# Optimization experiments

Measured on AMD Instinct MI355X. Metric: run time of the kernel, lower is better.

## Reference

```python
import jax, jax.numpy as jnp
import numpy as np

B, S, E, H, FFN, NQ = 4, 2048, 1024, 16, 4096, 8
DK = E // H
EPS = 1e-5


def setup_inputs() -> dict:
    key = jax.random.key(0)
    ks = jax.random.split(key, 8)
    x = jax.random.normal(ks[0], (B, S, E), dtype=jnp.float32)
    theta = jax.random.normal(ks[1], (NQ,), dtype=jnp.float32)  # RY angles
    w1 = jax.random.normal(ks[2], (FFN, NQ), dtype=jnp.float32) / np.sqrt(NQ)
    b1 = jnp.zeros((FFN,), dtype=jnp.float32)
    w2 = jax.random.normal(ks[3], (E, FFN), dtype=jnp.float32) / np.sqrt(FFN)
    b2 = jnp.zeros((E,), dtype=jnp.float32)
    gamma1 = jnp.ones((E,), dtype=jnp.float32)
    beta1 = jnp.zeros((E,), dtype=jnp.float32)
    gamma2 = jnp.ones((E,), dtype=jnp.float32)
    beta2 = jnp.zeros((E,), dtype=jnp.float32)
    return {"x": x, "theta": theta, "w1": w1, "b1": b1, "w2": w2, "b2": b2,
            "gamma1": gamma1, "beta1": beta1, "gamma2": gamma2, "beta2": beta2}


def _layernorm(h, g, b):
    mu = jnp.mean(h, axis=-1, keepdims=True)
    var = jnp.mean(jnp.square(h - mu), axis=-1, keepdims=True)
    return (h - mu) * jax.lax.rsqrt(var + EPS) * g + b


def _attention(x):
    # q = k = v = separate_heads(x); no projection weights in the original.
    q = x.reshape(B, S, H, DK).transpose(0, 2, 1, 3)  # [B,H,S,DK]
    scores = jnp.einsum("bhqd,bhkd->bhqk", q, q) / np.sqrt(DK)
    probs = jax.nn.softmax(scores, axis=-1)
    out = jnp.einsum("bhqk,bhkd->bhqd", probs, q)
    return out.transpose(0, 2, 1, 3).reshape(B, S, E)


def _ffn_quantum(h, theta, w1, b1, w2, b2):
    # Per-token circuit: RX(x_i) then RY(theta_i) on independent qubits,
    # measure PauliZ -> <Z_i> = cos(x_i) * cos(theta_i). Batched over all tokens.
    qout = jnp.cos(h[..., :NQ]) * jnp.cos(theta)  # [B,S,NQ]
    hid = jax.nn.relu(jnp.einsum("bsq,fq->bsf", qout, w1) + b1)
    return jnp.einsum("bsf,ef->bse", hid, w2) + b2


def reference(x, theta, w1, b1, w2, b2, gamma1, beta1, gamma2, beta2):
    attn_out = _attention(x)
    h = _layernorm(x + attn_out, gamma1, beta1)
    ffn_out = _ffn_quantum(h, theta, w1, b1, w2, b2)
    return _layernorm(h + ffn_out, gamma2, beta2)
```

## Files before the change

kernel.cpp:

```cpp
#include <hip/hip_runtime.h>


#define Bq 4
#define Sq 2048
#define Eq 1024
#define Hq 16
#define DKq 64
#define FFNq 4096
#define NQq 8
#define LOG2E 1.44269504f

typedef unsigned int u32;
typedef unsigned short u16;
typedef _Float16 f16;
typedef f16 f16x8 __attribute__((ext_vector_type(8)));
typedef __fp16 fp16x2 __attribute__((ext_vector_type(2)));
typedef float f32x4 __attribute__((ext_vector_type(4)));

#if __has_builtin(__builtin_amdgcn_exp2f)
#define EXP2F __builtin_amdgcn_exp2f
#else
#define EXP2F exp2f
#endif

#define MFMA(a, b, c) __builtin_amdgcn_mfma_f32_16x16x32_f16((a), (b), (c), 0, 0, 0)

#define GLL(g, l)                                                          \
  __builtin_amdgcn_global_load_lds(                                        \
      (const __attribute__((address_space(1))) u32*)(g),                   \
      (__attribute__((address_space(3))) u32*)(l), 16, 0, 0)

__device__ __forceinline__ u16 f2h(float x) {
  f16 t = (f16)x;
  return __builtin_bit_cast(u16, t);
}
__device__ __forceinline__ float h2f(u16 w) {
  return (float)__builtin_bit_cast(f16, w);
}
#if __has_builtin(__builtin_amdgcn_cvt_pkrtz)
__device__ __forceinline__ u32 pkrtz(float a, float b) {
  fp16x2 r = __builtin_amdgcn_cvt_pkrtz(a, b);
  return __builtin_bit_cast(u32, r);
}
#else
__device__ __forceinline__ u32 pkrtz(float a, float b) {
  return (u32)f2h(a) | ((u32)f2h(b) << 16);
}
#endif

union F8 { f16x8 v; u32 w[4]; u16 h[8]; f16 e[8]; };

__global__ void k_cvt(const float* __restrict__ src, uint4* __restrict__ dst, int n8) {
  int i = blockIdx.x * 256 + threadIdx.x;
  if (i >= n8) return;
  const float4* s = (const float4*)src + 2 * (long)i;
  float4 a = s[0], b = s[1];
  uint4 r;
  r.x = pkrtz(a.x, a.y);
  r.y = pkrtz(a.z, a.w);
  r.z = pkrtz(b.x, b.y);
  r.w = pkrtz(b.z, b.w);
  dst[i] = r;
}

__global__ void k_prep(const float* __restrict__ x, u16* __restrict__ xh,
                       u16* __restrict__ xt) {
  __shared__ u16 tile[64 * 72];
  const int tid = threadIdx.x;
  const int bx = blockIdx.x;
  const int sb = bx & 31, bh = bx >> 5;
  const int b = bh >> 4, h = bh & 15;
  const int s0 = sb * 64;
  const int r = tid >> 2, cq = tid & 3;
  const float* xp = x + ((long)(b * Sq + s0 + r)) * Eq + h * 64 + cq * 16;
  float4 f0 = ((const float4*)xp)[0], f1 = ((const float4*)xp)[1];
  float4 f2 = ((const float4*)xp)[2], f3 = ((const float4*)xp)[3];
  u32 w[8];
  w[0] = pkrtz(f0.x, f0.y); w[1] = pkrtz(f0.z, f0.w);
  w[2] = pkrtz(f1.x, f1.y); w[3] = pkrtz(f1.z, f1.w);
  w[4] = pkrtz(f2.x, f2.y); w[5] = pkrtz(f2.z, f2.w);
  w[6] = pkrtz(f3.x, f3.y); w[7] = pkrtz(f3.z, f3.w);
  uint4* xo = (uint4*)(xh + ((long)(b * Sq + s0 + r)) * Eq + h * 64 + cq * 16);
  xo[0] = make_uint4(w[0], w[1], w[2], w[3]);
  xo[1] = make_uint4(w[4], w[5], w[6], w[7]);
  uint4* tp = (uint4*)(tile + r * 72 + cq * 16);
  tp[0] = make_uint4(w[0], w[1], w[2], w[3]);
  tp[1] = make_uint4(w[4], w[5], w[6], w[7]);
  __syncthreads();
  const int d = tid >> 2, rq = tid & 3;
  u32 o[8];
#pragma unroll
  for (int i = 0; i < 8; ++i) {
    u32 lo = tile[(rq * 16 + 2 * i) * 72 + d];
    u32 hi = tile[(rq * 16 + 2 * i + 1) * 72 + d];
    o[i] = lo | (hi << 16);
  }
  uint4* to = (uint4*)(xt + ((long)(bh * 64 + d)) * Sq + s0 + rq * 16);
  to[0] = make_uint4(o[0], o[1], o[2], o[3]);
  to[1] = make_uint4(o[4], o[5], o[6], o[7]);
}

__global__ __launch_bounds__(256, 2) void k_attn(const u16* __restrict__ xh,
                                                 const u16* __restrict__ xt,
                                                 u16* __restrict__ attn) {
  __shared__ __align__(16) u16 lds[32768];
  u16* Pl = lds + 16384;

  const int tid = threadIdx.x;
  const int wave = tid >> 6, lane = tid & 63;
  const int n = lane & 15, quad = lane >> 4;

  const int bx = blockIdx.x;
  const int qb = bx >> 6, bh = bx & 63;
  const int b = bh >> 4, h = bh & 15;

  const u16* xh_bh = xh + (long)b * Sq * Eq + h * 64;
  const u16* xt_bh = xt + (long)bh * 64 * Sq;

  const float SC = 0.125f * LOG2E;
  F8 qf[4][2];
  float shift[4], lrow[4] = {0.f, 0.f, 0.f, 0.f};
#pragma unroll
  for (int nt = 0; nt < 4; ++nt) {
    const int q = qb * 256 + wave * 64 + nt * 16 + n;
    const u16* qp = xh_bh + (long)q * Eq + quad * 8;
    F8 a, c;
    a.v = *(const f16x8*)qp;
    c.v = *(const f16x8*)(qp + 32);
    float s2 = 0.f;
#pragma unroll
    for (int i = 0; i < 8; ++i) {
      float va = (float)a.e[i], vc = (float)c.e[i];
      s2 += va * va + vc * vc;
      qf[nt][0].e[i] = a.e[i] * (f16)SC;
      qf[nt][1].e[i] = c.e[i] * (f16)SC;
    }
    s2 += __shfl_xor(s2, 16);
    s2 += __shfl_xor(s2, 32);
    shift[nt] = SC * s2;
  }

  const int r8 = lane >> 3;
  const int cl = (lane & 7) ^ r8;
  const u16* gK0 = xh_bh + (long)(wave * 16 + r8) * Eq + cl * 8;
  const u16* gK1 = gK0 + 8 * Eq;
  const u16* gV0 = xt_bh + (long)(wave * 16 + r8) * Sq + cl * 8;
  const u16* gV1 = gV0 + 8 * Sq;
  const int lK0 = wave * 1024, lK1 = lK0 + 512;
  const int lV0 = 4096 + wave * 1024, lV1 = lV0 + 512;

  u16* cur = lds;
  u16* nxt = lds + 8192;

  GLL(gK0, cur + lK0); GLL(gK1, cur + lK1);
  GLL(gV0, cur + lV0); GLL(gV1, cur + lV1);
  gK0 += 64 * Eq; gK1 += 64 * Eq; gV0 += 64; gV1 += 64;

  f32x4 O[4][4] = {};
  u16* Pw = Pl + wave * 4096;

  for (int kb = 0; kb < Sq / 64; ++kb) {
    __syncthreads();
    if (kb < Sq / 64 - 1) {
      GLL(gK0, nxt + lK0); GLL(gK1, nxt + lK1);
      GLL(gV0, nxt + lV0); GLL(gV1, nxt + lV1);
      gK0 += 64 * Eq; gK1 += 64 * Eq; gV0 += 64; gV1 += 64;
    }
    u16* Kl = cur;
    u16* Vt = cur + 4096;

    f32x4 ST[4][4];
#pragma unroll
    for (int nt = 0; nt < 4; ++nt) {
      const float ms = -shift[nt];
#pragma unroll
      for (int mt = 0; mt < 4; ++mt) {
        ST[nt][mt][0] = ms; ST[nt][mt][1] = ms;
        ST[nt][mt][2] = ms; ST[nt][mt][3] = ms;
      }
    }
#pragma unroll
    for (int mt = 0; mt < 4; ++mt) {
#pragma unroll
      for (int c = 0; c < 2; ++c) {
        f16x8 af = *(const f16x8*)(Kl + (mt * 16 + n) * 64 +
                                   (((c * 4 + quad) ^ (n & 7)) * 8));
#pragma unroll
        for (int nt = 0; nt < 4; ++nt)
          ST[nt][mt] = MFMA(af, qf[nt][c].v, ST[nt][mt]);
      }
    }

#pragma unroll
    for (int nt = 0; nt < 4; ++nt) {
      float ls = 0.f;
#pragma unroll
      for (int mt = 0; mt < 4; ++mt) {
        float p0 = EXP2F(ST[nt][mt][0]);
        float p1 = EXP2F(ST[nt][mt][1]);
        float p2 = EXP2F(ST[nt][mt][2]);
        float p3 = EXP2F(ST[nt][mt][3]);
        ls += (p0 + p1) + (p2 + p3);
        const int ch = 2 * mt + (quad >> 1);
        *(uint2*)(Pw + nt * 1024 + n * 64 + ((ch ^ (n & 7)) * 8) + (quad & 1) * 4) =
            make_uint2(pkrtz(p0, p1), pkrtz(p2, p3));
      }
      lrow[nt] += ls;
    }

#pragma unroll
    for (int c = 0; c < 2; ++c) {
      const int pc = ((c * 4 + quad) ^ (n & 7)) * 8;
      f16x8 pf[4];
#pragma unroll
      for (int nt = 0; nt < 4; ++nt)
        pf[nt] = *(const f16x8*)(Pw + nt * 1024 + n * 64 + pc);
#pragma unroll
      for (int dt = 0; dt < 4; ++dt) {
        f16x8 vf = *(const f16x8*)(Vt + (dt * 16 + n) * 64 + pc);
#pragma unroll
        for (int nt = 0; nt < 4; ++nt) O[nt][dt] = MFMA(vf, pf[nt], O[nt][dt]);
      }
    }
    u16* t = cur; cur = nxt; nxt = t;
  }

#pragma unroll
  for (int nt = 0; nt < 4; ++nt) {
    float l = lrow[nt];
    l += __shfl_xor(l, 16);
    l += __shfl_xor(l, 32);
    const float inv = 1.0f / l;
    const int q = qb * 256 + wave * 64 + nt * 16 + n;
    u16* op = attn + (long)b * Sq * Eq + (long)q * Eq + h * 64;
#pragma unroll
    for (int dt = 0; dt < 4; ++dt) {
      u32 w0 = pkrtz(O[nt][dt][0] * inv, O[nt][dt][1] * inv);
      u32 w1 = pkrtz(O[nt][dt][2] * inv, O[nt][dt][3] * inv);
      *(uint2*)(op + dt * 16 + quad * 4) = make_uint2(w0, w1);
    }
  }
}

__global__ void k_ln1(const u16* __restrict__ xh, const u16* __restrict__ attn,
                      const float* __restrict__ g, const float* __restrict__ be,
                      const float* __restrict__ theta, u16* __restrict__ hout,
                      u16* __restrict__ qout) {
  const long t = blockIdx.x;
  const int tid = threadIdx.x;
  uint2 xw = ((const uint2*)(xh + t * Eq))[tid];
  uint2 aw = ((const uint2*)(attn + t * Eq))[tid];
  float v0 = h2f(xw.x & 0xffff) + h2f(aw.x & 0xffff);
  float v1 = h2f(xw.x >> 16) + h2f(aw.x >> 16);
  float v2 = h2f(xw.y & 0xffff) + h2f(aw.y & 0xffff);
  float v3 = h2f(xw.y >> 16) + h2f(aw.y >> 16);
  float s = (v0 + v1) + (v2 + v3);
  float s2 = v0 * v0 + v1 * v1 + v2 * v2 + v3 * v3;
#pragma unroll
  for (int o = 1; o < 64; o <<= 1) {
    s += __shfl_xor(s, o);
    s2 += __shfl_xor(s2, o);
  }
  __shared__ float red[8];
  const int wv = tid >> 6, ln = tid & 63;
  if (ln == 0) { red[wv] = s; red[4 + wv] = s2; }
  __syncthreads();
  s = red[0] + red[1] + red[2] + red[3];
  s2 = red[4] + red[5] + red[6] + red[7];
  const float mu = s * (1.f / Eq);
  const float var = s2 * (1.f / Eq) - mu * mu;
  const float rstd = rsqrtf(var + 1e-5f);
  float4 gv = ((const float4*)g)[tid];
  float4 bv = ((const float4*)be)[tid];
  float o0 = (v0 - mu) * rstd * gv.x + bv.x;
  float o1 = (v1 - mu) * rstd * gv.y + bv.y;
  float o2 = (v2 - mu) * rstd * gv.z + bv.z;
  float o3 = (v3 - mu) * rstd * gv.w + bv.w;
  ((uint2*)(hout + t * Eq))[tid] = make_uint2(pkrtz(o0, o1), pkrtz(o2, o3));
  if (tid < 2) {
    float hv[4] = {o0, o1, o2, o3};
    float q[4];
#pragma unroll
    for (int i = 0; i < 4; ++i) q[i] = cosf(hv[i]) * cosf(theta[tid * 4 + i]);
    *(uint2*)(qout + t * NQq + tid * 4) = make_uint2(pkrtz(q[0], q[1]), pkrtz(q[2], q[3]));
  }
}

__global__ void k_hid(const u16* __restrict__ qout, const float* __restrict__ w1,
                      const float* __restrict__ b1, u16* __restrict__ hid) {
  __shared__ float qs[256][8];
  const int tid = threadIdx.x;
  const int fb = blockIdx.x & 63, tb = blockIdx.x >> 6;
  const int f0 = fb * 64, t0 = tb * 256;
  {
    uint4 qw = *(const uint4*)(qout + (long)(t0 + tid) * NQq);
    qs[tid][0] = h2f(qw.x & 0xffff); qs[tid][1] = h2f(qw.x >> 16);
    qs[tid][2] = h2f(qw.y & 0xffff); qs[tid][3] = h2f(qw.y >> 16);
    qs[tid][4] = h2f(qw.z & 0xffff); qs[tid][5] = h2f(qw.z >> 16);
    qs[tid][6] = h2f(qw.w & 0xffff); qs[tid][7] = h2f(qw.w >> 16);
  }
  __syncthreads();
  const int wave = tid >> 6, lane = tid & 63;
  const int f = f0 + lane;
  const float4* wp = (const float4*)(w1 + (long)f * NQq);
  float4 wa = wp[0], wb = wp[1];
  const float bb = b1[f];
  const int trow = wave * 64;
  u16* op = hid + (long)(t0 + trow) * FFNq + f;
#pragma unroll 4
  for (int i = 0; i < 64; ++i) {
    const float* q = qs[trow + i];
    float acc = bb + q[0] * wa.x + q[1] * wa.y + q[2] * wa.z + q[3] * wa.w +
                q[4] * wb.x + q[5] * wb.y + q[6] * wb.z + q[7] * wb.w;
    acc = fmaxf(acc, 0.f);
    op[(long)i * FFNq] = f2h(acc);
  }
}

__global__ __launch_bounds__(256, 2) void k_gemm(const u16* __restrict__ Ah,
                                                 const u16* __restrict__ Bh,
                                                 u16* __restrict__ C) {
  __shared__ __align__(16) u16 lds[32768];
  const int tid = threadIdx.x;
  const int wave = tid >> 6, lane = tid & 63;
  const int n = lane & 15, quad = lane >> 4;
  const int wm = wave >> 1, wn = wave & 1;
  const int m0 = (blockIdx.x >> 3) * 128;
  const int n0 = (blockIdx.x & 7) * 128;
  const int r8 = lane >> 3;
  const int cl = (lane & 7) ^ r8;

  const u16* gA[4];
  const u16* gB[4];
  int lA[4], lB[4];
#pragma unroll
  for (int j = 0; j < 4; ++j) {
    const int row = wave * 32 + j * 8;
    gA[j] = Ah + (long)(m0 + row + r8) * FFNq + cl * 8;
    gB[j] = Bh + (long)(n0 + row + r8) * FFNq + cl * 8;
    lA[j] = row * 64;
    lB[j] = 8192 + row * 64;
  }

  u16* cur = lds;
  u16* nxt = lds + 16384;

#pragma unroll
  for (int j = 0; j < 4; ++j) {
    GLL(gA[j], cur + lA[j]);
    GLL(gB[j], cur + lB[j]);
    gA[j] += 64;
    gB[j] += 64;
  }

  f32x4 acc[4][4] = {};
  for (int it = 0; it < FFNq / 64; ++it) {
    __syncthreads();
    if (it < FFNq / 64 - 1) {
#pragma unroll
      for (int j = 0; j < 4; ++j) {
        GLL(gA[j], nxt + lA[j]);
        GLL(gB[j], nxt + lB[j]);
        gA[j] += 64;
        gB[j] += 64;
      }
    }
    u16* La = cur;
    u16* Lb = cur + 8192;
#pragma unroll
    for (int c = 0; c < 2; ++c) {
      f16x8 af[4], bf[4];
#pragma unroll
      for (int i = 0; i < 4; ++i) {
        const int ra = wm * 64 + i * 16 + n;
        const int rb = wn * 64 + i * 16 + n;
        af[i] = *(const f16x8*)(La + ra * 64 + (((c * 4 + quad) ^ (n & 7)) * 8));
        bf[i] = *(const f16x8*)(Lb + rb * 64 + (((c * 4 + quad) ^ (n & 7)) * 8));
      }
#pragma unroll
      for (int i = 0; i < 4; ++i)
#pragma unroll
        for (int j = 0; j < 4; ++j) acc[i][j] = MFMA(af[i], bf[j], acc[i][j]);
    }
    u16* t = cur; cur = nxt; nxt = t;
  }
#pragma unroll
  for (int i = 0; i < 4; ++i) {
    const int row = m0 + wm * 64 + i * 16 + quad * 4;
#pragma unroll
    for (int j = 0; j < 4; ++j) {
      u16* cp = C + (long)row * Eq + n0 + wn * 64 + j * 16 + n;
      cp[0] = f2h(acc[i][j][0]);
      cp[Eq] = f2h(acc[i][j][1]);
      cp[2 * Eq] = f2h(acc[i][j][2]);
      cp[3 * Eq] = f2h(acc[i][j][3]);
    }
  }
}

__global__ void k_ln2(const u16* __restrict__ hin, const u16* __restrict__ ffn,
                      const float* __restrict__ b2, const float* __restrict__ g,
                      const float* __restrict__ be, float* __restrict__ out) {
  const long t = blockIdx.x;
  const int tid = threadIdx.x;
  uint2 hw = ((const uint2*)(hin + t * Eq))[tid];
  uint2 fw = ((const uint2*)(ffn + t * Eq))[tid];
  float4 b2v = ((const float4*)b2)[tid];
  float v0 = h2f(hw.x & 0xffff) + h2f(fw.x & 0xffff) + b2v.x;
  float v1 = h2f(hw.x >> 16) + h2f(fw.x >> 16) + b2v.y;
  float v2 = h2f(hw.y & 0xffff) + h2f(fw.y & 0xffff) + b2v.z;
  float v3 = h2f(hw.y >> 16) + h2f(fw.y >> 16) + b2v.w;
  float s = (v0 + v1) + (v2 + v3);
  float s2 = v0 * v0 + v1 * v1 + v2 * v2 + v3 * v3;
#pragma unroll
  for (int o = 1; o < 64; o <<= 1) {
    s += __shfl_xor(s, o);
    s2 += __shfl_xor(s2, o);
  }
  __shared__ float red[8];
  const int wv = tid >> 6, ln = tid & 63;
  if (ln == 0) { red[wv] = s; red[4 + wv] = s2; }
  __syncthreads();
  s = red[0] + red[1] + red[2] + red[3];
  s2 = red[4] + red[5] + red[6] + red[7];
  const float mu = s * (1.f / Eq);
  const float var = s2 * (1.f / Eq) - mu * mu;
  const float rstd = rsqrtf(var + 1e-5f);
  float4 gv = ((const float4*)g)[tid];
  float4 bv = ((const float4*)be)[tid];
  float4 o;
  o.x = (v0 - mu) * rstd * gv.x + bv.x;
  o.y = (v1 - mu) * rstd * gv.y + bv.y;
  o.z = (v2 - mu) * rstd * gv.z + bv.z;
  o.w = (v3 - mu) * rstd * gv.w + bv.w;
  ((float4*)(out + t * Eq))[tid] = o;
}

extern "C" void kernel_launch(void* const* d_in, const int* in_sizes, int n_in,
                              void* d_out, int out_size, void* d_ws, size_t ws_size,
                              hipStream_t stream) {
  const float* x = (const float*)d_in[0];
  const float* theta = (const float*)d_in[1];
  const float* w1 = (const float*)d_in[2];
  const float* b1 = (const float*)d_in[3];
  const float* w2 = (const float*)d_in[4];
  const float* b2 = (const float*)d_in[5];
  const float* g1 = (const float*)d_in[6];
  const float* be1 = (const float*)d_in[7];
  const float* g2 = (const float*)d_in[8];
  const float* be2 = (const float*)d_in[9];
  float* out = (float*)d_out;

  char* ws = (char*)d_ws;
  u16* attn = (u16*)(ws);
  u16* h = (u16*)(ws + 16777216);
  u16* xh = (u16*)(ws + 33554432);
  u16* xt = (u16*)(ws + 50331648);
  u16* ffn = (u16*)(ws + 67108864);
  u16* hid = (u16*)(ws + 83886080);
  u16* w2h = (u16*)(ws + 150994944);
  u16* qout = (u16*)(ws + 159383552);

  k_prep<<<Bq * Hq * (Sq / 64), 256, 0, stream>>>(x, xh, xt);
  k_cvt<<<2048, 256, 0, stream>>>(w2, (uint4*)w2h, (Eq * FFNq) / 8);
  k_attn<<<Bq * Hq * (Sq / 256), 256, 0, stream>>>(xh, xt, attn);
  k_ln1<<<Bq * Sq, 256, 0, stream>>>(xh, attn, g1, be1, theta, h, qout);
  k_hid<<<(Bq * Sq / 256) * (FFNq / 64), 256, 0, stream>>>(qout, w1, b1, hid);
  k_gemm<<<(Bq * Sq / 128) * (Eq / 128), 256, 0, stream>>>(hid, w2h, ffn);
  k_ln2<<<Bq * Sq, 256, 0, stream>>>(h, ffn, b2, g2, be2, out);
}
```

Measured before the change: 316.9 us.

## Replace global_load_lds with register-staged prefetch and compute row sums via MFMA

Both the attention and FFN GEMM kernels stop using direct global-to-LDS loads. They now load the next tile into registers before the compute phase and write it to LDS after the compute, a classic register-staged double buffer. The attention kernel also drops the per-thread exp sum and the shuffle reductions, computing softmax row sums with an extra MFMA against a ones vector. This trades more registers, which may cut occupancy, and extra VALU/LDS store instructions for different load/compute overlap.

```diff
diff --git a/kernel.cpp b/kernel.cpp
--- a/kernel.cpp
+++ b/kernel.cpp
@@ -24,11 +24,6 @@
 #endif
 
 #define MFMA(a, b, c) __builtin_amdgcn_mfma_f32_16x16x32_f16((a), (b), (c), 0, 0, 0)
-
-#define GLL(g, l)                                                          \
-  __builtin_amdgcn_global_load_lds(                                        \
-      (const __attribute__((address_space(1))) u32*)(g),                   \
-      (__attribute__((address_space(3))) u32*)(l), 16, 0, 0)
 
 __device__ __forceinline__ u16 f2h(float x) {
   f16 t = (f16)x;
@@ -119,7 +114,7 @@
 
   const float SC = 0.125f * LOG2E;
   F8 qf[4][2];
-  float shift[4], lrow[4] = {0.f, 0.f, 0.f, 0.f};
+  float shift[4];
 #pragma unroll
   for (int nt = 0; nt < 4; ++nt) {
     const int q = qb * 256 + wave * 64 + nt * 16 + n;
@@ -146,24 +141,35 @@
   const u16* gK1 = gK0 + 8 * Eq;
   const u16* gV0 = xt_bh + (long)(wave * 16 + r8) * Sq + cl * 8;
   const u16* gV1 = gV0 + 8 * Sq;
-  const int lK0 = wave * 1024, lK1 = lK0 + 512;
-  const int lV0 = 4096 + wave * 1024, lV1 = lV0 + 512;
+  const int lK0 = wave * 1024 + lane * 8;
+  const int lK1 = lK0 + 512;
+  const int lV0 = 4096 + wave * 1024 + lane * 8;
+  const int lV1 = lV0 + 512;
 
   u16* cur = lds;
   u16* nxt = lds + 8192;
 
-  GLL(gK0, cur + lK0); GLL(gK1, cur + lK1);
-  GLL(gV0, cur + lV0); GLL(gV1, cur + lV1);
-  gK0 += 64 * Eq; gK1 += 64 * Eq; gV0 += 64; gV1 += 64;
+  {
+    uint4 sK0 = *(const uint4*)gK0, sK1 = *(const uint4*)gK1;
+    uint4 sV0 = *(const uint4*)gV0, sV1 = *(const uint4*)gV1;
+    gK0 += 64 * Eq; gK1 += 64 * Eq; gV0 += 64; gV1 += 64;
+    *(uint4*)(cur + lK0) = sK0; *(uint4*)(cur + lK1) = sK1;
+    *(uint4*)(cur + lV0) = sV0; *(uint4*)(cur + lV1) = sV1;
+  }
 
   f32x4 O[4][4] = {};
+  f32x4 lC[4] = {};
+  const f16x8 vones = {(f16)1, (f16)1, (f16)1, (f16)1,
+                       (f16)1, (f16)1, (f16)1, (f16)1};
   u16* Pw = Pl + wave * 4096;
 
   for (int kb = 0; kb < Sq / 64; ++kb) {
     __syncthreads();
-    if (kb < Sq / 64 - 1) {
-      GLL(gK0, nxt + lK0); GLL(gK1, nxt + lK1);
-      GLL(gV0, nxt + lV0); GLL(gV1, nxt + lV1);
+    const bool pre = kb < Sq / 64 - 1;
+    uint4 sK0, sK1, sV0, sV1;
+    if (pre) {
+      sK0 = *(const uint4*)gK0; sK1 = *(const uint4*)gK1;
+      sV0 = *(const uint4*)gV0; sV1 = *(const uint4*)gV1;
       gK0 += 64 * Eq; gK1 += 64 * Eq; gV0 += 64; gV1 += 64;
     }
     u16* Kl = cur;
@@ -193,19 +199,16 @@
 
 #pragma unroll
     for (int nt = 0; nt < 4; ++nt) {
-      float ls = 0.f;
 #pragma unroll
       for (int mt = 0; mt < 4; ++mt) {
         float p0 = EXP2F(ST[nt][mt][0]);
         float p1 = EXP2F(ST[nt][mt][1]);
         float p2 = EXP2F(ST[nt][mt][2]);
         float p3 = EXP2F(ST[nt][mt][3]);
-        ls += (p0 + p1) + (p2 + p3);
         const int ch = 2 * mt + (quad >> 1);
         *(uint2*)(Pw + nt * 1024 + n * 64 + ((ch ^ (n & 7)) * 8) + (quad & 1) * 4) =
             make_uint2(pkrtz(p0, p1), pkrtz(p2, p3));
       }
-      lrow[nt] += ls;
     }
 
 #pragma unroll
@@ -213,8 +216,10 @@
       const int pc = ((c * 4 + quad) ^ (n & 7)) * 8;
       f16x8 pf[4];
 #pragma unroll
-      for (int nt = 0; nt < 4; ++nt)
+      for (int nt = 0; nt < 4; ++nt) {
         pf[nt] = *(const f16x8*)(Pw + nt * 1024 + n * 64 + pc);
+        lC[nt] = MFMA(vones, pf[nt], lC[nt]);
+      }
 #pragma unroll
       for (int dt = 0; dt < 4; ++dt) {
         f16x8 vf = *(const f16x8*)(Vt + (dt * 16 + n) * 64 + pc);
@@ -222,15 +227,17 @@
         for (int nt = 0; nt < 4; ++nt) O[nt][dt] = MFMA(vf, pf[nt], O[nt][dt]);
       }
     }
+
+    if (pre) {
+      *(uint4*)(nxt + lK0) = sK0; *(uint4*)(nxt + lK1) = sK1;
+      *(uint4*)(nxt + lV0) = sV0; *(uint4*)(nxt + lV1) = sV1;
+    }
     u16* t = cur; cur = nxt; nxt = t;
   }
 
 #pragma unroll
   for (int nt = 0; nt < 4; ++nt) {
-    float l = lrow[nt];
-    l += __shfl_xor(l, 16);
-    l += __shfl_xor(l, 32);
-    const float inv = 1.0f / l;
+    const float inv = 1.0f / lC[nt][0];
     const int q = qb * 256 + wave * 64 + nt * 16 + n;
     u16* op = attn + (long)b * Sq * Eq + (long)q * Eq + h * 64;
 #pragma unroll
@@ -338,29 +345,39 @@
     const int row = wave * 32 + j * 8;
     gA[j] = Ah + (long)(m0 + row + r8) * FFNq + cl * 8;
     gB[j] = Bh + (long)(n0 + row + r8) * FFNq + cl * 8;
-    lA[j] = row * 64;
-    lB[j] = 8192 + row * 64;
+    lA[j] = row * 64 + lane * 8;
+    lB[j] = 8192 + row * 64 + lane * 8;
   }
 
   u16* cur = lds;
   u16* nxt = lds + 16384;
 
-#pragma unroll
-  for (int j = 0; j < 4; ++j) {
-    GLL(gA[j], cur + lA[j]);
-    GLL(gB[j], cur + lB[j]);
-    gA[j] += 64;
-    gB[j] += 64;
+  {
+    uint4 sA[4], sB[4];
+#pragma unroll
+    for (int j = 0; j < 4; ++j) {
+      sA[j] = *(const uint4*)gA[j];
+      sB[j] = *(const uint4*)gB[j];
+      gA[j] += 64;
+      gB[j] += 64;
+    }
+#pragma unroll
+    for (int j = 0; j < 4; ++j) {
+      *(uint4*)(cur + lA[j]) = sA[j];
+      *(uint4*)(cur + lB[j]) = sB[j];
+    }
   }
 
   f32x4 acc[4][4] = {};
   for (int it = 0; it < FFNq / 64; ++it) {
     __syncthreads();
-    if (it < FFNq / 64 - 1) {
+    const bool pre = it < FFNq / 64 - 1;
+    uint4 sA[4], sB[4];
+    if (pre) {
 #pragma unroll
       for (int j = 0; j < 4; ++j) {
-        GLL(gA[j], nxt + lA[j]);
-        GLL(gB[j], nxt + lB[j]);
+        sA[j] = *(const uint4*)gA[j];
+        sB[j] = *(const uint4*)gB[j];
         gA[j] += 64;
         gB[j] += 64;
       }
@@ -381,6 +398,13 @@
       for (int i = 0; i < 4; ++i)
 #pragma unroll
         for (int j = 0; j < 4; ++j) acc[i][j] = MFMA(af[i], bf[j], acc[i][j]);
+    }
+    if (pre) {
+#pragma unroll
+      for (int j = 0; j < 4; ++j) {
+        *(uint4*)(nxt + lA[j]) = sA[j];
+        *(uint4*)(nxt + lB[j]) = sB[j];
+      }
     }
     u16* t = cur; cur = nxt; nxt = t;
   }
```

New measurement: 425.6 us. 34.3% more time.

## Shrink attention query tile, split-K the FFN GEMM, single-buffer LDS

Applied to the files above, without the earlier changes.

The attention kernel now gives each block 128 queries instead of 256 and each wave 2 query tiles instead of 4. It drops the double-buffered K/V LDS staging in favor of a single buffer with two barriers per iteration, and computes softmax row sums with an extra MFMA against a vector of ones instead of scalar adds and shuffles. The FFN output GEMM is split along K into two halves that write separate partial buffers, and the second LayerNorm adds the two partials. The goal is to double the number of blocks and cut LDS and register use per block, raising occupancy and filling the CUs better. The cost is that global loads no longer overlap compute within a block, each iteration adds a barrier, and the GEMM writes and reads an extra fp16 partial buffer.

```diff
diff --git a/kernel.cpp b/kernel.cpp
--- a/kernel.cpp
+++ b/kernel.cpp
@@ -100,11 +100,13 @@
   to[1] = make_uint4(o[4], o[5], o[6], o[7]);
 }
 
-__global__ __launch_bounds__(256, 2) void k_attn(const u16* __restrict__ xh,
-                                                 const u16* __restrict__ xt,
-                                                 u16* __restrict__ attn) {
-  __shared__ __align__(16) u16 lds[32768];
-  u16* Pl = lds + 16384;
+__global__ __launch_bounds__(256) void k_attn(const u16* __restrict__ xh,
+                                              const u16* __restrict__ xt,
+                                              u16* __restrict__ attn) {
+  __shared__ __align__(16) u16 lds[16384];
+  u16* Kl = lds;
+  u16* Vt = lds + 4096;
+  u16* Pl = lds + 8192;
 
   const int tid = threadIdx.x;
   const int wave = tid >> 6, lane = tid & 63;
@@ -118,11 +120,11 @@
   const u16* xt_bh = xt + (long)bh * 64 * Sq;
 
   const float SC = 0.125f * LOG2E;
-  F8 qf[4][2];
-  float shift[4], lrow[4] = {0.f, 0.f, 0.f, 0.f};
-#pragma unroll
-  for (int nt = 0; nt < 4; ++nt) {
-    const int q = qb * 256 + wave * 64 + nt * 16 + n;
+  F8 qf[2][2];
+  float shift[2];
+#pragma unroll
+  for (int nt = 0; nt < 2; ++nt) {
+    const int q = qb * 128 + wave * 32 + nt * 16 + n;
     const u16* qp = xh_bh + (long)q * Eq + quad * 8;
     F8 a, c;
     a.v = *(const f16x8*)qp;
@@ -146,32 +148,28 @@
   const u16* gK1 = gK0 + 8 * Eq;
   const u16* gV0 = xt_bh + (long)(wave * 16 + r8) * Sq + cl * 8;
   const u16* gV1 = gV0 + 8 * Sq;
-  const int lK0 = wave * 1024, lK1 = lK0 + 512;
-  const int lV0 = 4096 + wave * 1024, lV1 = lV0 + 512;
-
-  u16* cur = lds;
-  u16* nxt = lds + 8192;
-
-  GLL(gK0, cur + lK0); GLL(gK1, cur + lK1);
-  GLL(gV0, cur + lV0); GLL(gV1, cur + lV1);
-  gK0 += 64 * Eq; gK1 += 64 * Eq; gV0 += 64; gV1 += 64;
-
-  f32x4 O[4][4] = {};
-  u16* Pw = Pl + wave * 4096;
+  u16* lK0 = Kl + wave * 1024;
+  u16* lK1 = lK0 + 512;
+  u16* lV0 = Vt + wave * 1024;
+  u16* lV1 = lV0 + 512;
+
+  f32x4 O[2][4] = {};
+  f32x4 lC[2] = {};
+  const f16x8 vones = {(f16)1, (f16)1, (f16)1, (f16)1,
+                       (f16)1, (f16)1, (f16)1, (f16)1};
+  u16* Pw0 = Pl + (wave * 2 + 0) * 1024;
+  u16* Pw1 = Pl + (wave * 2 + 1) * 1024;
 
   for (int kb = 0; kb < Sq / 64; ++kb) {
     __syncthreads();
-    if (kb < Sq / 64 - 1) {
-      GLL(gK0, nxt + lK0); GLL(gK1, nxt + lK1);
-      GLL(gV0, nxt + lV0); GLL(gV1, nxt + lV1);
-      gK0 += 64 * Eq; gK1 += 64 * Eq; gV0 += 64; gV1 += 64;
-    }
-    u16* Kl = cur;
-    u16* Vt = cur + 4096;
-
-    f32x4 ST[4][4];
-#pragma unroll
-    for (int nt = 0; nt < 4; ++nt) {
+    GLL(gK0, lK0); GLL(gK1, lK1);
+    GLL(gV0, lV0); GLL(gV1, lV1);
+    gK0 += 64 * Eq; gK1 += 64 * Eq; gV0 += 64; gV1 += 64;
+    __syncthreads();
+
+    f32x4 ST[2][4];
+#pragma unroll
+    for (int nt = 0; nt < 2; ++nt) {
       const float ms = -shift[nt];
 #pragma unroll
       for (int mt = 0; mt < 4; ++mt) {
@@ -185,53 +183,46 @@
       for (int c = 0; c < 2; ++c) {
         f16x8 af = *(const f16x8*)(Kl + (mt * 16 + n) * 64 +
                                    (((c * 4 + quad) ^ (n & 7)) * 8));
-#pragma unroll
-        for (int nt = 0; nt < 4; ++nt)
-          ST[nt][mt] = MFMA(af, qf[nt][c].v, ST[nt][mt]);
+        ST[0][mt] = MFMA(af, qf[0][c].v, ST[0][mt]);
+        ST[1][mt] = MFMA(af, qf[1][c].v, ST[1][mt]);
       }
     }
 
 #pragma unroll
-    for (int nt = 0; nt < 4; ++nt) {
-      float ls = 0.f;
+    for (int nt = 0; nt < 2; ++nt) {
+      u16* Pw = nt ? Pw1 : Pw0;
 #pragma unroll
       for (int mt = 0; mt < 4; ++mt) {
         float p0 = EXP2F(ST[nt][mt][0]);
         float p1 = EXP2F(ST[nt][mt][1]);
         float p2 = EXP2F(ST[nt][mt][2]);
         float p3 = EXP2F(ST[nt][mt][3]);
-        ls += (p0 + p1) + (p2 + p3);
         const int ch = 2 * mt + (quad >> 1);
-        *(uint2*)(Pw + nt * 1024 + n * 64 + ((ch ^ (n & 7)) * 8) + (quad & 1) * 4) =
+        *(uint2*)(Pw + n * 64 + ((ch ^ (n & 7)) * 8) + (quad & 1) * 4) =
             make_uint2(pkrtz(p0, p1), pkrtz(p2, p3));
       }
-      lrow[nt] += ls;
     }
 
 #pragma unroll
     for (int c = 0; c < 2; ++c) {
       const int pc = ((c * 4 + quad) ^ (n & 7)) * 8;
-      f16x8 pf[4];
-#pragma unroll
-      for (int nt = 0; nt < 4; ++nt)
-        pf[nt] = *(const f16x8*)(Pw + nt * 1024 + n * 64 + pc);
+      f16x8 pf0 = *(const f16x8*)(Pw0 + n * 64 + pc);
+      f16x8 pf1 = *(const f16x8*)(Pw1 + n * 64 + pc);
+      lC[0] = MFMA(vones, pf0, lC[0]);
+      lC[1] = MFMA(vones, pf1, lC[1]);
 #pragma unroll
       for (int dt = 0; dt < 4; ++dt) {
         f16x8 vf = *(const f16x8*)(Vt + (dt * 16 + n) * 64 + pc);
-#pragma unroll
-        for (int nt = 0; nt < 4; ++nt) O[nt][dt] = MFMA(vf, pf[nt], O[nt][dt]);
+        O[0][dt] = MFMA(vf, pf0, O[0][dt]);
+        O[1][dt] = MFMA(vf, pf1, O[1][dt]);
       }
     }
-    u16* t = cur; cur = nxt; nxt = t;
-  }
-
-#pragma unroll
-  for (int nt = 0; nt < 4; ++nt) {
-    float l = lrow[nt];
-    l += __shfl_xor(l, 16);
-    l += __shfl_xor(l, 32);
-    const float inv = 1.0f / l;
-    const int q = qb * 256 + wave * 64 + nt * 16 + n;
+  }
+
+#pragma unroll
+  for (int nt = 0; nt < 2; ++nt) {
+    const float inv = 1.0f / lC[nt][0];
+    const int q = qb * 128 + wave * 32 + nt * 16 + n;
     u16* op = attn + (long)b * Sq * Eq + (long)q * Eq + h * 64;
 #pragma unroll
     for (int dt = 0; dt < 4; ++dt) {
@@ -317,56 +308,50 @@
   }
 }
 
-__global__ __launch_bounds__(256, 2) void k_gemm(const u16* __restrict__ Ah,
-                                                 const u16* __restrict__ Bh,
-                                                 u16* __restrict__ C) {
-  __shared__ __align__(16) u16 lds[32768];
+__global__ __launch_bounds__(256) void k_gemm(const u16* __restrict__ Ah,
+                                              const u16* __restrict__ Bh,
+                                              u16* __restrict__ C0,
+                                              u16* __restrict__ C1) {
+  __shared__ __align__(16) u16 lds[16384];
+  u16* La = lds;
+  u16* Lb = lds + 8192;
   const int tid = threadIdx.x;
   const int wave = tid >> 6, lane = tid & 63;
   const int n = lane & 15, quad = lane >> 4;
   const int wm = wave >> 1, wn = wave & 1;
-  const int m0 = (blockIdx.x >> 3) * 128;
-  const int n0 = (blockIdx.x & 7) * 128;
+  const int bxx = blockIdx.x;
+  const int kk = bxx >> 9;
+  const int bx = bxx & 511;
+  const int m0 = (bx >> 3) * 128;
+  const int n0 = (bx & 7) * 128;
+  const int k0 = kk * (FFNq / 2);
   const int r8 = lane >> 3;
   const int cl = (lane & 7) ^ r8;
 
   const u16* gA[4];
   const u16* gB[4];
-  int lA[4], lB[4];
+  u16* lA[4];
+  u16* lB[4];
 #pragma unroll
   for (int j = 0; j < 4; ++j) {
     const int row = wave * 32 + j * 8;
-    gA[j] = Ah + (long)(m0 + row + r8) * FFNq + cl * 8;
-    gB[j] = Bh + (long)(n0 + row + r8) * FFNq + cl * 8;
-    lA[j] = row * 64;
-    lB[j] = 8192 + row * 64;
-  }
-
-  u16* cur = lds;
-  u16* nxt = lds + 16384;
-
-#pragma unroll
-  for (int j = 0; j < 4; ++j) {
-    GLL(gA[j], cur + lA[j]);
-    GLL(gB[j], cur + lB[j]);
-    gA[j] += 64;
-    gB[j] += 64;
+    gA[j] = Ah + (long)(m0 + row + r8) * FFNq + k0 + cl * 8;
+    gB[j] = Bh + (long)(n0 + row + r8) * FFNq + k0 + cl * 8;
+    lA[j] = La + row * 64;
+    lB[j] = Lb + row * 64;
   }
 
   f32x4 acc[4][4] = {};
-  for (int it = 0; it < FFNq / 64; ++it) {
+  for (int it = 0; it < FFNq / 2 / 64; ++it) {
     __syncthreads();
-    if (it < FFNq / 64 - 1) {
-#pragma unroll
-      for (int j = 0; j < 4; ++j) {
-        GLL(gA[j], nxt + lA[j]);
-        GLL(gB[j], nxt + lB[j]);
-        gA[j] += 64;
-        gB[j] += 64;
-      }
-    }
-    u16* La = cur;
-    u16* Lb = cur + 8192;
+#pragma unroll
+    for (int j = 0; j < 4; ++j) {
+      GLL(gA[j], lA[j]);
+      GLL(gB[j], lB[j]);
+      gA[j] += 64;
+      gB[j] += 64;
+    }
+    __syncthreads();
 #pragma unroll
     for (int c = 0; c < 2; ++c) {
       f16x8 af[4], bf[4];
@@ -382,8 +367,8 @@
 #pragma unroll
         for (int j = 0; j < 4; ++j) acc[i][j] = MFMA(af[i], bf[j], acc[i][j]);
     }
-    u16* t = cur; cur = nxt; nxt = t;
-  }
+  }
+  u16* C = kk ? C1 : C0;
 #pragma unroll
   for (int i = 0; i < 4; ++i) {
     const int row = m0 + wm * 64 + i * 16 + quad * 4;
@@ -398,18 +383,20 @@
   }
 }
 
-__global__ void k_ln2(const u16* __restrict__ hin, const u16* __restrict__ ffn,
-                      const float* __restrict__ b2, const float* __restrict__ g,
-                      const float* __restrict__ be, float* __restrict__ out) {
+__global__ void k_ln2(const u16* __restrict__ hin, const u16* __restrict__ p0f,
+                      const u16* __restrict__ p1f, const float* __restrict__ b2,
+                      const float* __restrict__ g, const float* __restrict__ be,
+                      float* __restrict__ out) {
   const long t = blockIdx.x;
   const int tid = threadIdx.x;
   uint2 hw = ((const uint2*)(hin + t * Eq))[tid];
-  uint2 fw = ((const uint2*)(ffn + t * Eq))[tid];
+  uint2 fw = ((const uint2*)(p0f + t * Eq))[tid];
+  uint2 ew = ((const uint2*)(p1f + t * Eq))[tid];
   float4 b2v = ((const float4*)b2)[tid];
-  float v0 = h2f(hw.x & 0xffff) + h2f(fw.x & 0xffff) + b2v.x;
-  float v1 = h2f(hw.x >> 16) + h2f(fw.x >> 16) + b2v.y;
-  float v2 = h2f(hw.y & 0xffff) + h2f(fw.y & 0xffff) + b2v.z;
-  float v3 = h2f(hw.y >> 16) + h2f(fw.y >> 16) + b2v.w;
+  float v0 = h2f(hw.x & 0xffff) + h2f(fw.x & 0xffff) + h2f(ew.x & 0xffff) + b2v.x;
+  float v1 = h2f(hw.x >> 16) + h2f(fw.x >> 16) + h2f(ew.x >> 16) + b2v.y;
+  float v2 = h2f(hw.y & 0xffff) + h2f(fw.y & 0xffff) + h2f(ew.y & 0xffff) + b2v.z;
+  float v3 = h2f(hw.y >> 16) + h2f(fw.y >> 16) + h2f(ew.y >> 16) + b2v.w;
   float s = (v0 + v1) + (v2 + v3);
   float s2 = v0 * v0 + v1 * v1 + v2 * v2 + v3 * v3;
 #pragma unroll
@@ -456,16 +443,17 @@
   u16* h = (u16*)(ws + 16777216);
   u16* xh = (u16*)(ws + 33554432);
   u16* xt = (u16*)(ws + 50331648);
-  u16* ffn = (u16*)(ws + 67108864);
-  u16* hid = (u16*)(ws + 83886080);
-  u16* w2h = (u16*)(ws + 150994944);
-  u16* qout = (u16*)(ws + 159383552);
+  u16* ffn0 = (u16*)(ws + 67108864);
+  u16* ffn1 = (u16*)(ws + 83886080);
+  u16* hid = (u16*)(ws + 100663296);
+  u16* w2h = (u16*)(ws + 167772160);
+  u16* qout = (u16*)(ws + 176160768);
 
   k_prep<<<Bq * Hq * (Sq / 64), 256, 0, stream>>>(x, xh, xt);
   k_cvt<<<2048, 256, 0, stream>>>(w2, (uint4*)w2h, (Eq * FFNq) / 8);
-  k_attn<<<Bq * Hq * (Sq / 256), 256, 0, stream>>>(xh, xt, attn);
+  k_attn<<<Bq * Hq * (Sq / 128), 256, 0, stream>>>(xh, xt, attn);
   k_ln1<<<Bq * Sq, 256, 0, stream>>>(xh, attn, g1, be1, theta, h, qout);
   k_hid<<<(Bq * Sq / 256) * (FFNq / 64), 256, 0, stream>>>(qout, w1, b1, hid);
-  k_gemm<<<(Bq * Sq / 128) * (Eq / 128), 256, 0, stream>>>(hid, w2h, ffn);
-  k_ln2<<<Bq * Sq, 256, 0, stream>>>(h, ffn, b2, g2, be2, out);
-}
+  k_gemm<<<2 * (Bq * Sq / 128) * (Eq / 128), 256, 0, stream>>>(hid, w2h, ffn0, ffn1);
+  k_ln2<<<Bq * Sq, 256, 0, stream>>>(h, ffn0, ffn1, b2, g2, be2, out);
+}
```

After: 348.0 us. 1.1x slower.
